# Performance work log

Hardware: AMD Instinct MI355X
Metric: run time of the kernel (lower is better)

Reference implementation:

```python
import jax, jax.numpy as jnp
import numpy as np

FAR = 10.0
RAST = 256          # rast_size default
ORIG_W, ORIG_H = 256.0, 256.0  # orig_size default
CHUNK = 32          # faces processed per scan step
EPS = 1e-9


def _project(vertices, K, R, t, dist):
    # persp projection with lens distortion; vertices [B,V,3] -> [B,V,3] (u,v in [-1,1], z depth)
    v = jnp.einsum('bvj,bij->bvi', vertices, R) + t
    x, y, z = v[..., 0], v[..., 1], v[..., 2]
    x_ = x / (z + EPS)
    y_ = y / (z + EPS)
    k1, k2, p1, p2, k3 = (dist[:, None, i] for i in range(5))
    r2 = x_ * x_ + y_ * y_  # == r**2 in original (r = sqrt(x_^2+y_^2))
    radial = 1.0 + k1 * r2 + k2 * r2 ** 2 + k3 * r2 ** 3
    x__ = x_ * radial + 2.0 * p1 * x_ * y_ + p2 * (r2 + 2.0 * x_ ** 2)
    y__ = y_ * radial + p1 * (r2 + 2.0 * y_ ** 2) + 2.0 * p2 * x_ * y_
    pts = jnp.stack([x__, y__, jnp.ones_like(z)], axis=-1)
    pts = jnp.einsum('bvj,bij->bvi', pts, K)
    u, vv = pts[..., 0], pts[..., 1]
    vv = ORIG_H - vv
    u = 2.0 * (u - ORIG_W / 2.0) / ORIG_W
    vv = 2.0 * (vv - ORIG_H / 2.0) / ORIG_H
    return jnp.stack([u, vv, z], axis=-1)


def _rasterize(fverts):
    # fverts: [B,F,3,3] per-face screen-space vertices (u,v,z). Z-buffer depth raster + coverage mask.
    B, F = fverts.shape[0], fverts.shape[1]
    pad = (-F) % CHUNK
    fv = jnp.pad(fverts, ((0, 0), (0, pad), (0, 0), (0, 0)))  # padded faces are degenerate (den==0)
    nc = (F + pad) // CHUNK
    fv = fv.reshape(B, nc, CHUNK, 3, 3).transpose(1, 0, 2, 3, 4)  # [nc,B,CHUNK,3,3]
    # pixel centers in [-1,1]; row i top-to-bottom maps to y = -1..1 (consistent with flipped v)
    g = 2.0 * (jnp.arange(RAST, dtype=jnp.float32) + 0.5) / RAST - 1.0
    X = g[None, None, None, :]   # cols
    Y = g[None, None, :, None]   # rows

    def body(carry, ch):
        zbuf, cover = carry
        e = lambda i, j: ch[:, :, i, j][:, :, None, None]
        ax, ay, az = e(0, 0), e(0, 1), e(0, 2)
        bx, by, bz = e(1, 0), e(1, 1), e(1, 2)
        cx, cy, cz = e(2, 0), e(2, 1), e(2, 2)
        den = (bx - ax) * (cy - ay) - (by - ay) * (cx - ax)
        ok = jnp.abs(den) > 1e-8
        den_s = jnp.where(ok, den, 1.0)
        # barycentric coords of each pixel wrt this face (signed; fill_back provides both windings)
        w0 = ((by - cy) * (X - cx) + (cx - bx) * (Y - cy)) / den_s
        w1 = ((cy - ay) * (X - cx) + (ax - cx) * (Y - cy)) / den_s
        w2 = 1.0 - w0 - w1
        zs = lambda zz: jnp.where(zz > 1e-8, zz, 1.0)
        inv = w0 / zs(az) + w1 / zs(bz) + w2 / zs(cz)  # perspective-correct 1/z interp
        valid = ok & (w0 >= 0) & (w1 >= 0) & (w2 >= 0)
        valid = valid & (az > 1e-8) & (bz > 1e-8) & (cz > 1e-8) & (inv > 1e-8)
        zp = 1.0 / jnp.where(valid, inv, 1.0)
        zc = jnp.min(jnp.where(valid, zp, FAR), axis=1)  # nearest face in this chunk [B,S,S]
        return (jnp.minimum(zbuf, zc), cover | jnp.any(valid, axis=1)), None

    zbuf0 = jnp.full((B, RAST, RAST), FAR, dtype=jnp.float32)
    cov0 = jnp.zeros((B, RAST, RAST), dtype=bool)
    (zbuf, cover), _ = jax.lax.scan(body, (zbuf0, cov0), fv)
    return zbuf, cover


def _normalize_depth(img, far):
    img_inf = (img == far).astype(jnp.float32)
    img_no_back = (1.0 - img_inf) * img
    img_max = img_no_back.max(axis=1, keepdims=True).max(axis=2, keepdims=True)
    img_min = img.min(axis=1, keepdims=True).min(axis=2, keepdims=True)
    nd = (img_max - img) / (img_max - img_min + 1e-4)
    return jnp.clip(nd, 0.0, 1.0)


def _forward(vertices, faces, intr, R, t, dist_coeffs):
    # fill_back=True: append faces with reversed vertex order
    faces_fb = jnp.concatenate([faces, faces[:, :, ::-1]], axis=1)
    uvz = _project(vertices, intr, R, t, dist_coeffs)
    fverts = jax.vmap(lambda v, f: v[f])(uvz, faces_fb)  # [B,F,3,3]
    zbuf, cover = _rasterize(fverts)
    dep = _normalize_depth(zbuf, FAR)
    mask = cover.astype(jnp.float32)
    return dep, mask


def setup_inputs():
    key = jax.random.key(0)
    k0, k1, k2 = jax.random.split(key, 3)
    B, V, F = 4, 778, 1538  # MANO hand mesh
    vertices = jax.random.normal(k0, (B, V, 3), dtype=jnp.float32) * 0.1 \
        + jnp.array([0.0, 0.0, 0.6], dtype=jnp.float32)  # blob 0.6m in front of camera
    faces = jax.random.randint(k1, (B, F, 3), 0, V, dtype=jnp.int32)
    K = jnp.tile(jnp.array([[500.0, 0.0, 128.0],
                            [0.0, 500.0, 128.0],
                            [0.0, 0.0, 1.0]], dtype=jnp.float32)[None], (B, 1, 1))
    R = jnp.tile(jnp.eye(3, dtype=jnp.float32)[None], (B, 1, 1))
    t = jnp.zeros((B, 1, 3), dtype=jnp.float32)
    dist_coeffs = jax.random.uniform(k2, (B, 5), dtype=jnp.float32) * 0.01
    return {"vertices": vertices, "faces": faces, "intr": K, "R": R, "t": t,
            "dist_coeffs": dist_coeffs}


def reference(vertices, faces, intr, R, t, dist_coeffs):
    return _forward(vertices, faces, intr, R, t, dist_coeffs)
```

## Files before the change

### kernel.cpp

```cpp
#include <hip/hip_runtime.h>
#include <cstdint>

#define RASTN 256
#define FARV 10.0f
#define FARBITS 0x41200000u
#define SPLIT 4
#define NBUCK 1024
#define NINITY 8

__device__ __forceinline__ float gval(int i) {
    return (2.0f * ((float)i + 0.5f)) / 256.0f - 1.0f;
}

__global__ __launch_bounds__(1024) void prep_sort_kernel(
    const float* __restrict__ verts, const int* __restrict__ faces,
    const float* __restrict__ Km, const float* __restrict__ Rm,
    const float* __restrict__ tm, const float* __restrict__ dm,
    float4* __restrict__ rec, uint2* __restrict__ sax, unsigned short* __restrict__ stri,
    unsigned int* __restrict__ zbits, unsigned int* __restrict__ mm,
    float* __restrict__ uvzg, int V, int F, int F2, int F2c, int B, int npix)
{
#pragma clang fp contract(off)
    __shared__ float s_uvz[1024*3];
    __shared__ unsigned int s_pk[4096];
    __shared__ unsigned short s_bk[4096];
    __shared__ unsigned int s_hist[NBUCK], s_cnt2[NBUCK];
    __shared__ unsigned int s_ws[16];
    int b = blockIdx.x, y = blockIdx.y, tid = threadIdx.x;
    int lane = tid & 63, wv16 = tid >> 6;
    uint4* zb4 = (uint4*)(zbits + (size_t)b * npix);
    int n4 = npix >> 2;
    int sl0 = (n4 * y) / NINITY, sl1 = (n4 * (y + 1)) / NINITY;
    for (int i = sl0 + tid; i < sl1; i += 1024)
        zb4[i] = make_uint4(FARBITS, FARBITS, FARBITS, FARBITS);
    if (y > 0) return;
    if (tid == 0) { mm[2*b] = 0u; mm[2*b+1] = FARBITS; }
    for (int i = tid; i < NBUCK; i += 1024) s_hist[i] = 0u;
    int seg = F2c / SPLIT;
    uint2* sxb = sax + (size_t)b * F2c;
    unsigned short* stb = stri + (size_t)b * F2c;
    for (int p = F2 + tid; p < F2c; p += 1024) {
        int addr = (p % SPLIT) * seg + p / SPLIT;
        sxb[addr] = make_uint2(1u , __float_as_uint(3e38f));
        stb[addr] = 0;
    }
    bool inlds = (V <= 1024);
    const float* R = Rm + b*9; const float* K = Km + b*9;
    const float* t = tm + b*3; const float* d = dm + b*5;
    for (int v = tid; v < V; v += 1024) {
        float vx = verts[((size_t)b*V + v)*3+0];
        float vy = verts[((size_t)b*V + v)*3+1];
        float vz = verts[((size_t)b*V + v)*3+2];
        float cxm = ((vx*R[0] + vy*R[1]) + vz*R[2]) + t[0];
        float cym = ((vx*R[3] + vy*R[4]) + vz*R[5]) + t[1];
        float czm = ((vx*R[6] + vy*R[7]) + vz*R[8]) + t[2];
        float zd = czm + 1e-9f;
        float x_ = cxm / zd;
        float y_ = cym / zd;
        float k1 = d[0], k2 = d[1], p1 = d[2], p2 = d[3], k3 = d[4];
        float r2   = (x_*x_) + (y_*y_);
        float r2_2 = r2 * r2;
        float r2_3 = r2 * r2_2;
        float radial = ((1.0f + k1*r2) + k2*r2_2) + k3*r2_3;
        float x__ = ((x_*radial) + (((2.0f*p1)*x_)*y_)) + (p2*(r2 + 2.0f*(x_*x_)));
        float y__ = ((y_*radial) + (p1*(r2 + 2.0f*(y_*y_)))) + (((2.0f*p2)*x_)*y_);
        float up = ((x__*K[0]) + (y__*K[1])) + (1.0f*K[2]);
        float vp = ((x__*K[3]) + (y__*K[4])) + (1.0f*K[5]);
        vp = 256.0f - vp;
        float un = (2.0f*(up - 128.0f)) / 256.0f;
        float vn = (2.0f*(vp - 128.0f)) / 256.0f;
        if (inlds) { s_uvz[v*3+0]=un; s_uvz[v*3+1]=vn; s_uvz[v*3+2]=czm; }
        else { uvzg[((size_t)b*V+v)*3+0]=un; uvzg[((size_t)b*V+v)*3+1]=vn; uvzg[((size_t)b*V+v)*3+2]=czm; }
    }
    __syncthreads();
    const float* ub = inlds ? s_uvz : (uvzg + (size_t)b*V*3);
    const int* fb = faces + (size_t)b * F * 3;
    float4* rb = rec + (size_t)b * F2 * 4;
    bool stash = (F2 <= 4096);
    for (int j = tid; j < F2; j += 1024) {
        int i0, i1, i2;
        if (j < F) { i0 = fb[j*3+0]; i1 = fb[j*3+1]; i2 = fb[j*3+2]; }
        else { int jj = j - F; i0 = fb[jj*3+2]; i1 = fb[jj*3+1]; i2 = fb[jj*3+0]; }
        float ax = ub[i0*3+0], ay = ub[i0*3+1], az = ub[i0*3+2];
        float bx = ub[i1*3+0], by = ub[i1*3+1], bz = ub[i1*3+2];
        float cx = ub[i2*3+0], cy = ub[i2*3+1], cz = ub[i2*3+2];
        float den = (bx-ax)*(cy-ay) - (by-ay)*(cx-ax);
        bool ok = fabsf(den) > 1e-8f;
        float dens = ok ? den : 1.0f;
        bool alive = ok && (az > 1e-8f) && (bz > 1e-8f) && (cz > 1e-8f);
        float za = (az > 1e-8f) ? az : 1.0f;
        float zb = (bz > 1e-8f) ? bz : 1.0f;
        float zc = (cz > 1e-8f) ? cz : 1.0f;
        float mnx = fminf(ax, fminf(bx, cx));
        float mxx = fmaxf(ax, fmaxf(bx, cx));
        float mny = fminf(ay, fminf(by, cy));
        float mxy = fmaxf(ay, fmaxf(by, cy));
        float m = 1e-3f + 1e-6f*((fabsf(mnx)+fabsf(mxx))+(fabsf(mny)+fabsf(mxy)));
        mnx -= m; mxx += m; mny -= m; mxy += m;
        if (!(mxx >= -1.0f) || !(mnx <= 1.0f) || !(mxy >= -1.0f) || !(mny <= 1.0f)) alive = false;
        int ic0 = 1, ic1 = 0, ir0 = 1, ir1 = 0;
        float minz = 3e38f;
        if (alive) {
            float lx = fmaxf(mnx, -1.5f), hx = fminf(mxx, 1.5f);
            float ly = fmaxf(mny, -1.5f), hy = fminf(mxy, 1.5f);
            ic0 = (int)floorf((lx + 1.0f) * 128.0f - 0.5f);
            ic1 = (int)ceilf ((hx + 1.0f) * 128.0f - 0.5f);
            ir0 = (int)floorf((ly + 1.0f) * 128.0f - 0.5f);
            ir1 = (int)ceilf ((hy + 1.0f) * 128.0f - 0.5f);
            ic0 = ic0 < 0 ? 0 : ic0;  ir0 = ir0 < 0 ? 0 : ir0;
            ic1 = ic1 > 255 ? 255 : ic1;  ir1 = ir1 > 255 ? 255 : ir1;
            if (ic0 > ic1 || ir0 > ir1) { ic0 = 1; ic1 = 0; ir0 = 1; ir1 = 0; minz = 3e38f; }
            else minz = fminf(za, fminf(zb, zc)) * (1.0f - 4e-4f);
        }
        float minzv = fminf(za, fminf(zb, zc));
        float maxzv = fmaxf(za, fmaxf(zb, zc));
        float a0 = by - cy, b0 = cx - bx;
        float a1 = cy - ay, b1 = ax - cx;
        float densf = dens;
        if (dens < 0.0f) { a0 = -a0; b0 = -b0; a1 = -a1; b1 = -b1; densf = -dens; }
        float rd = __builtin_amdgcn_rcpf(densf);
        float ra, rbz, rc;
        if (minzv > 1e-2f && maxzv < 100.0f * minzv) {
            ra  = __builtin_amdgcn_rcpf(za);
            rbz = __builtin_amdgcn_rcpf(zb);
            rc  = __builtin_amdgcn_rcpf(zc);
        } else {
            ra = rbz = rc = __builtin_huge_valf();
        }
        unsigned int pack = (unsigned int)(ic0 | (ic1 << 8) | (ir0 << 16) | (ir1 << 24));
        int bk = NBUCK - 1;
        if (minz < 1e30f) {
            bk = (int)(minz * 512.0f);
            bk = bk < 0 ? 0 : (bk > NBUCK-2 ? NBUCK-2 : bk);
        }
        size_t base = (size_t)j * 4;
        rb[base+0] = make_float4(cx, cy, a0, b0);
        rb[base+1] = make_float4(a1, b1, densf, rd);
        rb[base+2] = make_float4(ra, rbz, rc, minz);
        rb[base+3] = make_float4(__uint_as_float(pack), za, zb, zc);
        atomicAdd(&s_hist[bk], 1u);
        if (stash) { s_pk[j] = pack; s_bk[j] = (unsigned short)bk; }
    }
    __syncthreads();
    {
        unsigned int h = s_hist[tid];
        unsigned int v = h;
        for (int o = 1; o < 64; o <<= 1) {
            unsigned int tsh = __shfl_up(v, o, 64);
            if (lane >= o) v += tsh;
        }
        if (lane == 63) s_ws[wv16] = v;
        __syncthreads();
        if (tid < 16) {
            unsigned int w = s_ws[tid];
            for (int o = 1; o < 16; o <<= 1) {
                unsigned int tsh = __shfl_up(w, o, 64);
                if (tid >= o) w += tsh;
            }
            s_ws[tid] = w;
        }
        __syncthreads();
        unsigned int add = (wv16 > 0) ? s_ws[wv16 - 1] : 0u;
        s_cnt2[tid] = v + add - h;
    }
    __syncthreads();
    for (int j = tid; j < F2; j += 1024) {
        unsigned int pack; int bk;
        if (stash) { pack = s_pk[j]; bk = (int)s_bk[j]; }
        else {
            float4 q3 = rb[(size_t)j*4+3];
            float4 q2 = rb[(size_t)j*4+2];
            pack = __float_as_uint(q3.x);
            float mz = q2.w;
            bk = NBUCK - 1;
            if (mz < 1e30f) { bk = (int)(mz * 512.0f); bk = bk < 0 ? 0 : (bk > NBUCK-2 ? NBUCK-2 : bk); }
        }
        float key = (bk == NBUCK-1) ? 3e38f : (float)bk * (1.0f/512.0f);
        int pos = (int)atomicAdd(&s_cnt2[bk], 1u);
        int addr = (pos % SPLIT) * seg + pos / SPLIT;
        sxb[addr] = make_uint2(pack, __float_as_uint(key));
        stb[addr] = (unsigned short)j;
    }
}

__global__ __launch_bounds__(256) void raster_kernel(
    const float4* __restrict__ rec, const uint2* __restrict__ sax,
    const unsigned short* __restrict__ stri, unsigned int* __restrict__ zbits,
    int F2, int F2c)
{
#pragma clang fp contract(off)
    __shared__ float4 sh[256];
    __shared__ float2 s_kb[256];
    __shared__ unsigned short s_list[256];
    __shared__ int s_wk[4], s_kk[4], s_wo[4];
    __shared__ int s_tot, s_kc;
    __shared__ float s_tzmax, s_red[4];
    int zz = blockIdx.z;
    int b = zz / SPLIT, sp = zz - b*SPLIT;
    int tc = blockIdx.x, tr = blockIdx.y;
    int tid = threadIdx.x, lane = tid & 63, wv = tid >> 6;
    int tx = tid & 15, ty = tid >> 4;
    int col = tc*16 + tx, row = tr*16 + ty;
    float X = gval(col), Y = gval(row);
    int pc0 = tc*16, pc1 = pc0+15, pr0 = tr*16, pr1 = pr0+15;
    int wvs = __builtin_amdgcn_readfirstlane(wv);
    int wr0 = pr0 + wvs*4, wr1 = wr0 + 3;
    float Xc = 0.5f*(gval(pc0) + gval(pc1));
    float Yc = 0.5f*(gval(pr0) + gval(pr1));
    const float hxr = 15.0f/256.0f, hyr = 15.0f/256.0f;
    int seg = F2c / SPLIT;
    const float4* rb = rec + (size_t)b * F2 * 4;
    const uint2* sxb = sax + (size_t)b * F2c + (size_t)sp * seg;
    const unsigned short* stb = stri + (size_t)b * F2c + (size_t)sp * seg;
    size_t pix = ((size_t)b*RASTN + row)*RASTN + col;
    unsigned int* zp_g = zbits + pix;
    float zmin = FARV;
    float pushed = FARV;
    if (tid == 0) s_tzmax = FARV;
    __syncthreads();
    int nch = (seg + 255) / 256;
    for (int c = 0; c < nch; ++c) {
        int s = c*256 + tid;
        bool kp = false, sv = false; unsigned int tri = 0; float kf = 0.0f;
        unsigned int pkv = 0;
        if (s < seg) {
            uint2 a = sxb[s];
            kf = __uint_as_float(a.y);
            kp = !(kf > s_tzmax);
            if (kp) {
                int pk = (int)a.x;
                int ic0 = pk & 255, ic1 = (pk >> 8) & 255;
                int ir0 = (pk >> 16) & 255, ir1 = (pk >> 24) & 255;
                sv = (ic0 <= ic1) && (ic0 <= pc1) && (ic1 >= pc0) && (ir0 <= pr1) && (ir1 >= pr0);
                if (sv) {
                    tri = stb[s];
                    pkv = a.x;
                    float4 q0 = rb[(size_t)tri*4 + 0];
                    float4 q1 = rb[(size_t)tri*4 + 1];
                    float4 q2 = rb[(size_t)tri*4 + 2];
                    float a0 = q0.z, b0 = q0.w;
                    float a1 = q1.x, b1 = q1.y;
                    float xcd = Xc - q0.x, ycd = Yc - q0.y;
                    float e0c = (a0*xcd) + (b0*ycd);
                    float e1c = (a1*xcd) + (b1*ycd);
                    float den = q1.z;
                    float e2c = (den - e0c) - e1c;
                    float a2 = -(a0 + a1), b2 = -(b0 + b1);
                    float t0 = fabsf(a0)*hxr + fabsf(b0)*hyr;
                    float t1 = fabsf(a1)*hxr + fabsf(b1)*hyr;
                    float t2 = fabsf(a2)*hxr + fabsf(b2)*hyr;
                    float m0 = e0c + t0;
                    float m1 = e1c + t1;
                    float m2 = e2c + t2;
                    bool cull = (m0 < -1e-5f*(fabsf(e0c) + t0 + 1.0f))
                             || (m1 < -1e-5f*(fabsf(e1c) + t1 + 1.0f))
                             || (m2 < -1e-5f*(fabsf(e2c) + t2 + 1.0f));
                    if (cull) sv = false;
                    else {
                        float e0m = fmaxf(m0, 0.0f);
                        float e1m = fmaxf(m1, 0.0f);
                        float e2m = fmaxf(m2, 0.0f);
                        float S = ((e0m*q2.x) + (e1m*q2.y)) + (e2m*q2.z);
                        S = S * (1.0f + 2e-3f);
                        float zlb = (den * __builtin_amdgcn_rcpf(S)) * (1.0f - 2e-3f);
                        if (zlb > s_tzmax) sv = false;
                    }
                }
            }
        }
        unsigned long long bs = __ballot(sv ? 1 : 0);
        unsigned long long bk = __ballot(kp ? 1 : 0);
        int pfx = __popcll(bs & ((1ull << lane) - 1ull));
        if (lane == 0) { s_wk[wv] = __popcll(bs); s_kk[wv] = __popcll(bk); }
        __syncthreads();
        if (tid == 0) {
            int acc = 0;
            for (int q = 0; q < 4; ++q) { s_wo[q] = acc; acc += s_wk[q]; }
            s_tot = acc;
            s_kc = s_kk[0] + s_kk[1] + s_kk[2] + s_kk[3];
        }
        __syncthreads();
        if (sv) {
            int pos = s_wo[wv] + pfx;
            s_list[pos] = (unsigned short)tri;
            s_kb[pos] = make_float2(kf, __uint_as_float(pkv));
        }
        int kcnt = s_kc, n = s_tot;
        if (kcnt == 0) break;
        for (int g = 0; g < n; g += 64) {
            __syncthreads();
            float zg = __uint_as_float(__hip_atomic_load(
                zp_g, __ATOMIC_RELAXED, __HIP_MEMORY_SCOPE_AGENT));
            float2 kbv = s_kb[g + lane];
            int cnt2 = (n - g) < 64 ? (n - g) : 64;
            if (tid < cnt2*4) {
                unsigned int t4 = s_list[g + (tid >> 2)];
                sh[tid] = rb[(size_t)t4*4 + (tid & 3)];
            }
            __syncthreads();
            pushed = fminf(pushed, zg);
            zmin = fminf(zmin, zg);
            int vkey = __float_as_int(kbv.x);
            int vbb  = __float_as_int(kbv.y);
            for (int i = 0; i < cnt2; ++i) {
                float ky = __int_as_float(__builtin_amdgcn_readlane(vkey, i));
                if (ky > zmin) break;
                unsigned int pk = (unsigned int)__builtin_amdgcn_readlane(vbb, i);
                int ir0 = (int)((pk >> 16) & 255u), ir1 = (int)(pk >> 24);
                if (ir1 < wr0 || ir0 > wr1) continue;
                int ic0 = (int)(pk & 255u), ic1 = (int)((pk >> 8) & 255u);
                if (col < ic0 || col > ic1 || row < ir0 || row > ir1) continue;
                float4 q0 = sh[i*4+0];
                float4 q1 = sh[i*4+1];
                float xc = X - q0.x;
                float yc = Y - q0.y;
                float e0 = (q0.z*xc) + (q0.w*yc);
                float e1 = (q1.x*xc) + (q1.y*yc);
                float rd = q1.w;
                float w0a = e0*rd, w1a = e1*rd;
                float w2a = (1.0f - w0a) - w1a;
                float epsu = 1e-4f*((1.0f + fabsf(w0a)) + fabsf(w1a));
                if (e0 > -1e-30f && e1 > -1e-30f && w2a > -epsu) {
                    float4 q2 = sh[i*4+2];
                    float inva = ((w0a*q2.x) + (w1a*q2.y)) + (w2a*q2.z);
                    float zpa = __builtin_amdgcn_rcpf(inva);
                    bool clearly = (e0 > 0.0f) && (e1 > 0.0f) && (w2a > epsu) && (inva > 1e-6f);
                    if (!clearly || zpa < zmin*1.001f) {
                        float4 q3 = sh[i*4+3];
                        float dens = q1.z;
                        float w0 = e0 / dens;
                        float w1 = e1 / dens;
                        float w2 = (1.0f - w0) - w1;
                        float inv = ((w0 / q3.y) + (w1 / q3.z)) + (w2 / q3.w);
                        if ((w0 >= 0.0f) && (w1 >= 0.0f) && (w2 >= 0.0f) && (inv > 1e-8f)) {
                            float zp = 1.0f / inv;
                            zmin = fminf(zmin, zp);
                        }
                    }
                }
            }
            if (zmin < pushed) {
                atomicMin(zp_g, __float_as_uint(zmin));
                pushed = zmin;
            }
        }
        if (n > 0) {
            float zx = zmin;
            for (int o = 32; o; o >>= 1) zx = fmaxf(zx, __shfl_xor(zx, o));
            if (lane == 0) s_red[wv] = zx;
        }
        __syncthreads();
        if (n > 0 && tid == 0)
            s_tzmax = fminf(s_tzmax,
                fmaxf(fmaxf(s_red[0], s_red[1]), fmaxf(s_red[2], s_red[3])));
        __syncthreads();
    }
    if (zmin < pushed)
        atomicMin(zp_g, __float_as_uint(zmin));
}

__global__ __launch_bounds__(256) void minmax_kernel(
    const float4* __restrict__ zbuf, float4* __restrict__ mask,
    unsigned int* __restrict__ mm, int npix)
{
    __shared__ float smx[4], smn[4];
    int b = blockIdx.y;
    size_t i4 = (((size_t)b * npix) >> 2) + (size_t)blockIdx.x * 256 + threadIdx.x;
    float4 z = zbuf[i4];
    float4 mk;
    mk.x = (z.x < FARV) ? 1.0f : 0.0f;
    mk.y = (z.y < FARV) ? 1.0f : 0.0f;
    mk.z = (z.z < FARV) ? 1.0f : 0.0f;
    mk.w = (z.w < FARV) ? 1.0f : 0.0f;
    mask[i4] = mk;
    float nbx = (z.x == FARV) ? 0.0f : z.x;
    float nby = (z.y == FARV) ? 0.0f : z.y;
    float nbz = (z.z == FARV) ? 0.0f : z.z;
    float nbw = (z.w == FARV) ? 0.0f : z.w;
    float vmx = fmaxf(fmaxf(nbx, nby), fmaxf(nbz, nbw));
    float vmn = fminf(fminf(z.x, z.y), fminf(z.z, z.w));
    int lane = threadIdx.x & 63, wv = threadIdx.x >> 6;
    for (int o = 32; o; o >>= 1) {
        vmx = fmaxf(vmx, __shfl_xor(vmx, o));
        vmn = fminf(vmn, __shfl_xor(vmn, o));
    }
    if (lane == 0) { smx[wv] = vmx; smn[wv] = vmn; }
    __syncthreads();
    if (threadIdx.x == 0) {
        float bmx = fmaxf(fmaxf(smx[0], smx[1]), fmaxf(smx[2], smx[3]));
        float bmn = fminf(fminf(smn[0], smn[1]), fminf(smn[2], smn[3]));
        atomicMax(mm + 2*b,     __float_as_uint(bmx));
        atomicMin(mm + 2*b + 1, __float_as_uint(bmn));
    }
}

__global__ __launch_bounds__(256) void final_kernel(
    float4* __restrict__ zdep, const unsigned int* __restrict__ mm,
    int npix4, int total4)
{
#pragma clang fp contract(off)
    int idx = blockIdx.x*256 + threadIdx.x;
    if (idx >= total4) return;
    int b = idx / npix4;
    float mx = __uint_as_float(mm[2*b]);
    float mn = __uint_as_float(mm[2*b + 1]);
    float den = (mx - mn) + 1e-4f;
    float4 z = zdep[idx];
    float4 r;
    r.x = (mx - z.x) / den;
    r.y = (mx - z.y) / den;
    r.z = (mx - z.z) / den;
    r.w = (mx - z.w) / den;
    r.x = r.x < 0.0f ? 0.0f : (r.x > 1.0f ? 1.0f : r.x);
    r.y = r.y < 0.0f ? 0.0f : (r.y > 1.0f ? 1.0f : r.y);
    r.z = r.z < 0.0f ? 0.0f : (r.z > 1.0f ? 1.0f : r.z);
    r.w = r.w < 0.0f ? 0.0f : (r.w > 1.0f ? 1.0f : r.w);
    zdep[idx] = r;
}

extern "C" void kernel_launch(void* const* d_in, const int* in_sizes, int n_in,
                              void* d_out, int out_size, void* d_ws, size_t ws_size,
                              hipStream_t stream)
{
    const float* verts = (const float*)d_in[0];
    const int*   faces = (const int*)d_in[1];
    const float* Km    = (const float*)d_in[2];
    const float* Rm    = (const float*)d_in[3];
    const float* tm    = (const float*)d_in[4];
    const float* dm    = (const float*)d_in[5];
    float* out = (float*)d_out;

    int B  = in_sizes[2] / 9;
    int V  = in_sizes[0] / (3 * B);
    int F  = in_sizes[1] / (3 * B);
    int F2 = 2 * F;
    int F2c = ((F2 + SPLIT - 1) / SPLIT) * SPLIT;
    int npix = RASTN * RASTN;

    char* ws = (char*)d_ws;
    size_t off = 0;
    float4* rec = (float4*)(ws + off);
    off = (off + (size_t)B * F2 * 4 * sizeof(float4) + 255) & ~(size_t)255;
    uint2* sax = (uint2*)(ws + off);
    off = (off + (size_t)B * F2c * sizeof(uint2) + 255) & ~(size_t)255;
    unsigned short* stri = (unsigned short*)(ws + off);
    off = (off + (size_t)B * F2c * sizeof(unsigned short) + 255) & ~(size_t)255;
    float* uvzg = (float*)(ws + off);
    off = (off + (size_t)B * V * 3 * sizeof(float) + 255) & ~(size_t)255;
    unsigned int* mm = (unsigned int*)(ws + off);

    unsigned int* zbits = (unsigned int*)out;
    float* mask = out + (size_t)B * npix;

    dim3 pgrid(B, NINITY);
    prep_sort_kernel<<<pgrid, 1024, 0, stream>>>(
        verts, faces, Km, Rm, tm, dm, rec, sax, stri, zbits, mm, uvzg,
        V, F, F2, F2c, B, npix);
    dim3 rgrid(16, 16, B * SPLIT);
    raster_kernel<<<rgrid, 256, 0, stream>>>(rec, sax, stri, zbits, F2, F2c);
    dim3 mgrid(npix / 1024, B);
    minmax_kernel<<<mgrid, 256, 0, stream>>>(
        (const float4*)zbits, (float4*)mask, mm, npix);
    int npix4 = npix >> 2;
    int total4 = B * npix4;
    final_kernel<<<(total4 + 255) / 256, 256, 0, stream>>>(
        (float4*)zbits, mm, npix4, total4);
}
```

Before: 160.3 us.

## Fuse min/max reduction and depth normalization via per-batch grid barrier

Merges the min/max reduction kernel and the final normalization kernel into one launch. Blocks of the same batch sync through an atomic arrival counter with a spin-wait, then read the reduced min/max and normalize the z values they already hold in registers. This removes one kernel launch and a second global read of the depth buffer. The spin barrier needs all 256 blocks co-resident to avoid deadlock, which holds at this grid size but is not guaranteed in general.

```diff
diff --git a/kernel.cpp b/kernel.cpp
--- a/kernel.cpp
+++ b/kernel.cpp
@@ -18,6 +18,7 @@
     const float* __restrict__ tm, const float* __restrict__ dm,
     float4* __restrict__ rec, uint2* __restrict__ sax, unsigned short* __restrict__ stri,
     unsigned int* __restrict__ zbits, unsigned int* __restrict__ mm,
+    unsigned int* __restrict__ cnt,
     float* __restrict__ uvzg, int V, int F, int F2, int F2c, int B, int npix)
 {
 #pragma clang fp contract(off)
@@ -34,7 +35,7 @@
     for (int i = sl0 + tid; i < sl1; i += 1024)
         zb4[i] = make_uint4(FARBITS, FARBITS, FARBITS, FARBITS);
     if (y > 0) return;
-    if (tid == 0) { mm[2*b] = 0u; mm[2*b+1] = FARBITS; }
+    if (tid == 0) { mm[2*b] = 0u; mm[2*b+1] = FARBITS; cnt[b] = 0u; }
     for (int i = tid; i < NBUCK; i += 1024) s_hist[i] = 0u;
     int seg = F2c / SPLIT;
     uint2* sxb = sax + (size_t)b * F2c;
@@ -359,14 +360,16 @@
         atomicMin(zp_g, __float_as_uint(zmin));
 }
 
-__global__ __launch_bounds__(256) void minmax_kernel(
-    const float4* __restrict__ zbuf, float4* __restrict__ mask,
-    unsigned int* __restrict__ mm, int npix)
+__global__ __launch_bounds__(256) void minmax_final_kernel(
+    float4* __restrict__ zdep, float4* __restrict__ mask,
+    unsigned int* __restrict__ mm, unsigned int* __restrict__ cnt, int npix)
 {
+#pragma clang fp contract(off)
     __shared__ float smx[4], smn[4];
     int b = blockIdx.y;
+    int nb = gridDim.x;
     size_t i4 = (((size_t)b * npix) >> 2) + (size_t)blockIdx.x * 256 + threadIdx.x;
-    float4 z = zbuf[i4];
+    float4 z = zdep[i4];
     float4 mk;
     mk.x = (z.x < FARV) ? 1.0f : 0.0f;
     mk.y = (z.y < FARV) ? 1.0f : 0.0f;
@@ -391,21 +394,21 @@
         float bmn = fminf(fminf(smn[0], smn[1]), fminf(smn[2], smn[3]));
         atomicMax(mm + 2*b,     __float_as_uint(bmx));
         atomicMin(mm + 2*b + 1, __float_as_uint(bmn));
-    }
-}
-
-__global__ __launch_bounds__(256) void final_kernel(
-    float4* __restrict__ zdep, const unsigned int* __restrict__ mm,
-    int npix4, int total4)
-{
-#pragma clang fp contract(off)
-    int idx = blockIdx.x*256 + threadIdx.x;
-    if (idx >= total4) return;
-    int b = idx / npix4;
-    float mx = __uint_as_float(mm[2*b]);
-    float mn = __uint_as_float(mm[2*b + 1]);
+        asm volatile("s_waitcnt vmcnt(0)" ::: "memory");
+        __hip_atomic_fetch_add(&cnt[b], 1u,
+            __ATOMIC_RELAXED, __HIP_MEMORY_SCOPE_AGENT);
+        while (__hip_atomic_load(&cnt[b],
+                __ATOMIC_RELAXED, __HIP_MEMORY_SCOPE_AGENT) < (unsigned int)nb)
+            __builtin_amdgcn_s_sleep(7);
+    }
+    __syncthreads();
+    unsigned int mxb = __hip_atomic_load(mm + 2*b,
+        __ATOMIC_RELAXED, __HIP_MEMORY_SCOPE_AGENT);
+    unsigned int mnb = __hip_atomic_load(mm + 2*b + 1,
+        __ATOMIC_RELAXED, __HIP_MEMORY_SCOPE_AGENT);
+    float mx = __uint_as_float(mxb);
+    float mn = __uint_as_float(mnb);
     float den = (mx - mn) + 1e-4f;
-    float4 z = zdep[idx];
     float4 r;
     r.x = (mx - z.x) / den;
     r.y = (mx - z.y) / den;
@@ -415,7 +418,7 @@
     r.y = r.y < 0.0f ? 0.0f : (r.y > 1.0f ? 1.0f : r.y);
     r.z = r.z < 0.0f ? 0.0f : (r.z > 1.0f ? 1.0f : r.z);
     r.w = r.w < 0.0f ? 0.0f : (r.w > 1.0f ? 1.0f : r.w);
-    zdep[idx] = r;
+    zdep[i4] = r;
 }
 
 extern "C" void kernel_launch(void* const* d_in, const int* in_sizes, int n_in,
@@ -448,21 +451,18 @@
     float* uvzg = (float*)(ws + off);
     off = (off + (size_t)B * V * 3 * sizeof(float) + 255) & ~(size_t)255;
     unsigned int* mm = (unsigned int*)(ws + off);
+    unsigned int* cnt = mm + 2 * B;
 
     unsigned int* zbits = (unsigned int*)out;
     float* mask = out + (size_t)B * npix;
 
     dim3 pgrid(B, NINITY);
     prep_sort_kernel<<<pgrid, 1024, 0, stream>>>(
-        verts, faces, Km, Rm, tm, dm, rec, sax, stri, zbits, mm, uvzg,
+        verts, faces, Km, Rm, tm, dm, rec, sax, stri, zbits, mm, cnt, uvzg,
         V, F, F2, F2c, B, npix);
     dim3 rgrid(16, 16, B * SPLIT);
     raster_kernel<<<rgrid, 256, 0, stream>>>(rec, sax, stri, zbits, F2, F2c);
-    dim3 mgrid(npix / 1024, B);
-    minmax_kernel<<<mgrid, 256, 0, stream>>>(
-        (const float4*)zbits, (float4*)mask, mm, npix);
-    int npix4 = npix >> 2;
-    int total4 = B * npix4;
-    final_kernel<<<(total4 + 255) / 256, 256, 0, stream>>>(
-        (float4*)zbits, mm, npix4, total4);
+    dim3 fgrid(npix / 1024, B);
+    minmax_final_kernel<<<fgrid, 256, 0, stream>>>(
+        (float4*)zbits, (float4*)mask, mm, cnt, npix);
 }
```

New measurement: 163.5 us. 1.02x slower.
